# Kernel optimization log

Measured on AMD Instinct MI355X. Metric: run time of the kernel, lower is better.

Reference implementation:

```python
import jax, jax.numpy as jnp
import numpy as np

N = 50000        # number of amino_acid nodes
E = 250000       # edges per relation
HID = 64         # resid_hidden_dim (per-head out dim)
H = 4            # num_heads
L = 2            # resid_num_layers
IN_DIM = 256     # input_dim (fc_dim output)
SCALE = 1.0 / np.sqrt(HID)
EPS_BN = 1e-5


def setup_inputs() -> dict:
    key = jax.random.key(0)
    ks = jax.random.split(key, 12)
    inp = {"x": jax.random.normal(ks[0], (N, HID), jnp.float32)}
    for i, nm in enumerate(("seq", "knn", "dis")):
        inp[f"src_{nm}"] = jax.random.randint(ks[1 + 2 * i], (E,), 0, N, dtype=jnp.int32)
        inp[f"dst_{nm}"] = jax.random.randint(ks[2 + 2 * i], (E,), 0, N, dtype=jnp.int32)
    s = 0.05
    inp["Wsrc"] = jax.random.normal(ks[7], (L, 3, HID, H * HID), jnp.float32) * s
    inp["Wdst"] = jax.random.normal(ks[8], (L, 3, HID, H * HID), jnp.float32) * s
    inp["Wfc"] = jax.random.normal(ks[9], (L, HID, HID), jnp.float32) * s
    inp["bfc"] = jnp.zeros((L, HID), jnp.float32)
    inp["gamma"] = jnp.ones((L, HID), jnp.float32)
    inp["beta"] = jnp.zeros((L, HID), jnp.float32)
    inp["Wdim"] = jax.random.normal(ks[10], (HID, IN_DIM), jnp.float32) * s
    inp["bdim"] = jnp.zeros((IN_DIM,), jnp.float32)
    return inp


def _gat_dot(x, Wsrc, Wdst, src, dst):
    # GATDotConv: q/k projections, scaled dot-product attention per edge,
    # edge-softmax over incoming edges per destination, sum aggregation.
    fs = (x @ Wsrc).reshape(N, H, HID)   # key/value (source) features
    fd = (x @ Wdst).reshape(N, H, HID)   # query (destination) features
    e = jnp.einsum("ehd,ehd->eh", fs[src], fd[dst]) * SCALE   # [E, H]
    m = jax.ops.segment_max(e, dst, num_segments=N)           # [N, H]
    m = jnp.where(jnp.isfinite(m), m, 0.0)                    # zero-in-degree safe
    p = jnp.exp(e - m[dst])
    denom = jax.ops.segment_sum(p, dst, num_segments=N)       # [N, H]
    alpha = p / jnp.maximum(denom[dst], 1e-9)                 # [E, H]
    return jax.ops.segment_sum(fs[src] * alpha[:, :, None], dst, num_segments=N)  # [N, H, HID]


def _batchnorm(x, gamma, beta):
    mu = jnp.mean(x, axis=0)
    var = jnp.var(x, axis=0)
    return gamma * (x - mu) * jax.lax.rsqrt(var + EPS_BN) + beta


def reference(x, src_seq, dst_seq, src_knn, dst_knn, src_dis, dst_dis,
              Wsrc, Wdst, Wfc, bfc, gamma, beta, Wdim, bdim):
    edges = ((src_seq, dst_seq), (src_knn, dst_knn), (src_dis, dst_dis))
    h = x
    for l in range(L):
        # HeteroGraphConv with aggregate='sum' over the three relations
        agg = jnp.zeros((N, H, HID), h.dtype)
        for r in range(3):
            agg = agg + _gat_dot(h, Wsrc[l, r], Wdst[l, r], edges[r][0], edges[r][1])
        h = jnp.mean(agg, axis=1)                       # mean over heads -> [N, HID]
        h = _batchnorm(jax.nn.relu(h @ Wfc[l] + bfc[l]), gamma[l], beta[l])
        # dropout omitted (identity in eval / deterministic reference)
    return h @ Wdim + bdim                              # [N, IN_DIM]
```

## Files before the change

kernel.cpp:

```cpp
#include <hip/hip_runtime.h>
#include <math.h>

#define N_NODES 50000
#define E_EDGES 250000
#define HID 64
#define HD 256
#define L_LAYERS 2
#define IN_DIM_ 256
#define ATT_SCALE 0.125f
#define LOG2E 1.44269504f
#define EPS_BN 1e-5f
#define GX 782

#define PACK_REL (6 * 512 * 64)
#define PACK_FC  (2 * 64 * 64)
#define PACK_DIM (256 * 64)
#define HIST_B   2930
#define PACK_B   864
#define CVT_B    3125
#define PROJ_B   (GX * 3)

#define NBUCK 782
#define P2_B  (3 * NBUCK)
#define BCSTR 32
#define BCAP  512

#define TS 72

typedef __attribute__((ext_vector_type(8))) short bf16x8;
typedef __attribute__((ext_vector_type(4))) float f32x4;

static __device__ __forceinline__ unsigned short f2bf(float f) {
    unsigned u = __float_as_uint(f);
    unsigned r = (u + 0x7fff + ((u >> 16) & 1)) >> 16;
    return (unsigned short)r;
}
static __device__ __forceinline__ float bf2f(unsigned u) {
    return __uint_as_float(u << 16);
}

static __device__ __forceinline__ float rowsum16(float x) {
    int t;
    t = __builtin_amdgcn_update_dpp(0, __float_as_int(x), 0xB1, 0xf, 0xf, true);
    x += __int_as_float(t);
    t = __builtin_amdgcn_update_dpp(0, __float_as_int(x), 0x4E, 0xf, 0xf, true);
    x += __int_as_float(t);
    t = __builtin_amdgcn_update_dpp(0, __float_as_int(x), 0x141, 0xf, 0xf, true);
    x += __int_as_float(t);
    t = __builtin_amdgcn_update_dpp(0, __float_as_int(x), 0x140, 0xf, 0xf, true);
    x += __int_as_float(t);
    return x;
}


__global__ __launch_bounds__(256) void u1_kernel(
        const int* __restrict__ s0, const int* __restrict__ d0,
        const int* __restrict__ s1, const int* __restrict__ d1,
        const int* __restrict__ s2, const int* __restrict__ d2,
        int* __restrict__ bcur, unsigned* __restrict__ ebuf,
        const float* __restrict__ Wsrc, const float* __restrict__ Wdst,
        const float* __restrict__ Wfc, const float* __restrict__ Wdim,
        unsigned short* __restrict__ WtRel, unsigned short* __restrict__ WtFc,
        unsigned short* __restrict__ WtDim,
        const float* __restrict__ x, unsigned short* __restrict__ xb) {
    int b = blockIdx.x;
    if (b < HIST_B) {
        int i = b * 256 + threadIdx.x;
        if (i < 3 * E_EDGES) {
            int r = i / E_EDGES;
            int e = i - r * E_EDGES;
            const int* src = (r == 0) ? s0 : ((r == 1) ? s1 : s2);
            const int* dst = (r == 0) ? d0 : ((r == 1) ? d1 : d2);
            int d = dst[e], s = src[e];
            int bk = r * NBUCK + (d >> 6);
            int pos = atomicAdd(&bcur[(size_t)bk * BCSTR], 1);
            if (pos < BCAP)
                ebuf[(size_t)bk * BCAP + pos] = (unsigned)d | ((unsigned)s << 16);
        }
    } else if (b < HIST_B + PACK_B) {
        int i = (b - HIST_B) * 256 + threadIdx.x;
        if (i < PACK_REL) {
            int k = i & 63;
            int n = (i >> 6) & 511;
            int lr = i >> 15;
            const float* srcm = (n < 256) ? Wsrc : Wdst;
            WtRel[i] = f2bf(srcm[((size_t)lr * 64 + k) * 256 + (n & 255)]);
        } else if (i < PACK_REL + PACK_FC) {
            int j = i - PACK_REL;
            int l = j >> 12, rem = j & 4095;
            int k = rem & 63, n = rem >> 6;
            WtFc[j] = f2bf(Wfc[(size_t)l * 4096 + k * 64 + n]);
        } else if (i < PACK_REL + PACK_FC + PACK_DIM) {
            int j = i - PACK_REL - PACK_FC;
            int k = j & 63, n = j >> 6;
            WtDim[j] = f2bf(Wdim[(size_t)k * 256 + n]);
        }
    } else {
        int i = ((b - HIST_B - PACK_B) * 256 + threadIdx.x) * 4;
        if (i < N_NODES * HID) {
            float4 v = *(const float4*)(x + i);
            uint2 o;
            o.x = (unsigned)f2bf(v.x) | ((unsigned)f2bf(v.y) << 16);
            o.y = (unsigned)f2bf(v.z) | ((unsigned)f2bf(v.w) << 16);
            *(uint2*)(xb + i) = o;
        }
    }
}


__global__ __launch_bounds__(1024) void bscan_kernel(const int* __restrict__ bcur,
                                                     int* __restrict__ bstart,
                                                     int* __restrict__ row_off) {
    __shared__ int A[1024], B[1024];
    int tid = threadIdx.x;
    int r = blockIdx.x;
    int v = (tid < NBUCK) ? bcur[(size_t)(r * NBUCK + tid) * BCSTR] : 0;
    if (v > BCAP) v = BCAP;
    A[tid] = v;
    __syncthreads();
    int* s = A; int* d = B;
    for (int o = 1; o < 1024; o <<= 1) {
        int x = s[tid];
        if (tid >= o) x += s[tid - o];
        d[tid] = x;
        __syncthreads();
        int* t = s; s = d; d = t;
    }
    if (tid < NBUCK) bstart[r * NBUCK + tid] = s[tid] - v;
    if (tid == 0) row_off[(size_t)r * (N_NODES + 1) + N_NODES] = E_EDGES;
}


static __device__ __forceinline__ void proj_body8(int bx,
        const unsigned short* __restrict__ hB, const unsigned short* __restrict__ Wt,
        unsigned short* __restrict__ out, int M, unsigned short* tile) {
    int tid = threadIdx.x;
    int wave = tid >> 6, lane = tid & 63;
    int q = lane >> 4, li = lane & 15;
    int nodeLoc = (wave >> 1) * 32;
    int featLoc = (wave & 1) * 32;
    int nodeBase = bx * 64 + nodeLoc;

    bf16x8 bfr[2][2];
    #pragma unroll
    for (int t = 0; t < 2; ++t) {
        int node = nodeBase + t * 16 + li; if (node >= M) node = M - 1;
        const unsigned short* bp = hB + (size_t)node * 64 + q * 8;
        #pragma unroll
        for (int s = 0; s < 2; ++s) bfr[t][s] = *(const bf16x8*)(bp + s * 32);
    }

    #pragma unroll
    for (int py = 0; py < 8; ++py) {
        int featBase = py * 64 + featLoc;
        bf16x8 afr[2][2];
        #pragma unroll
        for (int t = 0; t < 2; ++t) {
            const unsigned short* ap = Wt + (size_t)(featBase + t * 16 + li) * 64 + q * 8;
            #pragma unroll
            for (int s = 0; s < 2; ++s) afr[t][s] = *(const bf16x8*)(ap + s * 32);
        }
        f32x4 acc[2][2];
        #pragma unroll
        for (int a = 0; a < 2; ++a)
            #pragma unroll
            for (int bq = 0; bq < 2; ++bq)
                #pragma unroll
                for (int i = 0; i < 4; ++i) acc[a][bq][i] = 0.f;
        #pragma unroll
        for (int s = 0; s < 2; ++s)
            #pragma unroll
            for (int ft = 0; ft < 2; ++ft)
                #pragma unroll
                for (int nt = 0; nt < 2; ++nt)
                    acc[ft][nt] = __builtin_amdgcn_mfma_f32_16x16x32_bf16(afr[ft][s], bfr[nt][s], acc[ft][nt], 0, 0, 0);

        #pragma unroll
        for (int ft = 0; ft < 2; ++ft) {
            int fl = featLoc + ft * 16 + q * 4;
            #pragma unroll
            for (int nt = 0; nt < 2; ++nt) {
                int nl = nodeLoc + nt * 16 + li;
                unsigned lo = (unsigned)f2bf(acc[ft][nt][0]) | ((unsigned)f2bf(acc[ft][nt][1]) << 16);
                unsigned hi = (unsigned)f2bf(acc[ft][nt][2]) | ((unsigned)f2bf(acc[ft][nt][3]) << 16);
                uint2 pk; pk.x = lo; pk.y = hi;
                *(uint2*)(tile + nl * TS + fl) = pk;
            }
        }
        __syncthreads();
        #pragma unroll
        for (int p = 0; p < 2; ++p) {
            int idx = p * 256 + tid;
            int nl = idx >> 3, sg = idx & 7;
            int node = bx * 64 + nl;
            if (node < M) {
                uint4 v = *(const uint4*)(tile + nl * TS + sg * 8);
                *(uint4*)(out + (size_t)node * 512 + py * 64 + sg * 8) = v;
            }
        }
        __syncthreads();
    }
}


__global__ __launch_bounds__(256) void u2b_kernel(
        const int* __restrict__ bstart, const int* __restrict__ bcur,
        const unsigned* __restrict__ ebuf, int* __restrict__ csr_src,
        int* __restrict__ row_off,
        const unsigned short* __restrict__ xb, const unsigned short* __restrict__ WtRel0,
        unsigned short* __restrict__ p0, unsigned short* __restrict__ p1,
        unsigned short* __restrict__ p2) {
    __shared__ __align__(16) unsigned short tile[64 * TS];
    __shared__ int cnt64[64], cur64[64];
    int b = blockIdx.x;
    int tid = threadIdx.x;
    if (b < P2_B) {
        int r = b / NBUCK, bk = b - r * NBUCK;
        int n0 = bk << 6;
        int base = bstart[r * NBUCK + bk];
        int cnt = bcur[(size_t)(r * NBUCK + bk) * BCSTR];
        if (cnt > BCAP) cnt = BCAP;
        if (tid < 64) cnt64[tid] = 0;
        __syncthreads();
        const unsigned* eb = ebuf + (size_t)(r * NBUCK + bk) * BCAP;
        for (int t = tid; t < cnt; t += 256)
            atomicAdd(&cnt64[(eb[t] & 0xffff) - n0], 1);
        __syncthreads();
        if (tid < 64) {
            int x = cnt64[tid];
            int incl = x;
            #pragma unroll
            for (int o = 1; o < 64; o <<= 1) {
                int y = __shfl_up(incl, o, 64);
                if (tid >= o) incl += y;
            }
            int excl = incl - x;
            cur64[tid] = excl;
            int node = n0 + tid;
            if (node < N_NODES)
                row_off[(size_t)r * (N_NODES + 1) + node] = base + excl;
        }
        __syncthreads();
        int* cs = csr_src + (size_t)r * E_EDGES + base;
        for (int t = tid; t < cnt; t += 256) {
            unsigned v = eb[t];
            int d = (v & 0xffff) - n0;
            int s = (int)(v >> 16);
            int pos = atomicAdd(&cur64[d], 1);
            cs[pos] = s;
        }
    } else {
        int b2 = b - P2_B;
        int px = b2 % GX;
        int pz = b2 / GX;
        unsigned short* out = (pz == 0) ? p0 : ((pz == 1) ? p1 : p2);
        proj_body8(px, xb, WtRel0 + (size_t)pz * 512 * 64, out, N_NODES, tile);
    }
}

__global__ __launch_bounds__(256) void gemm_proj3(const unsigned short* __restrict__ hB,
                                                  const unsigned short* __restrict__ WtL,
                                                  unsigned short* __restrict__ p0,
                                                  unsigned short* __restrict__ p1,
                                                  unsigned short* __restrict__ p2,
                                                  int M) {
    __shared__ __align__(16) unsigned short tile[64 * TS];
    int r = blockIdx.z;
    unsigned short* out = (r == 0) ? p0 : ((r == 1) ? p1 : p2);
    proj_body8(blockIdx.x, hB, WtL + (size_t)r * 512 * 64, out, M, tile);
}

__global__ __launch_bounds__(256) void gemm_f32out(const unsigned short* __restrict__ hB,
                                                   const unsigned short* __restrict__ Wt,
                                                   const float* __restrict__ bias,
                                                   float* __restrict__ out,
                                                   int M, int Nout, int relu) {
    int tid = threadIdx.x;
    int wave = tid >> 6, lane = tid & 63;
    int q = lane >> 4, li = lane & 15;
    int nodeBase = blockIdx.x * 64 + (wave >> 1) * 32;
    int featBase = blockIdx.y * 64 + (wave & 1) * 32;

    const unsigned short* aptr[2];
    const unsigned short* bptr[2];
    #pragma unroll
    for (int t = 0; t < 2; ++t) {
        aptr[t] = Wt + (size_t)(featBase + t * 16 + li) * 64 + q * 8;
        int node = nodeBase + t * 16 + li; if (node >= M) node = M - 1;
        bptr[t] = hB + (size_t)node * 64 + q * 8;
    }
    f32x4 acc[2][2];
    #pragma unroll
    for (int a = 0; a < 2; ++a)
        #pragma unroll
        for (int bq = 0; bq < 2; ++bq)
            #pragma unroll
            for (int i = 0; i < 4; ++i) acc[a][bq][i] = 0.f;

    #pragma unroll
    for (int s = 0; s < 2; ++s) {
        bf16x8 a[2], b[2];
        #pragma unroll
        for (int t = 0; t < 2; ++t) {
            a[t] = *(const bf16x8*)(aptr[t] + s * 32);
            b[t] = *(const bf16x8*)(bptr[t] + s * 32);
        }
        #pragma unroll
        for (int ft = 0; ft < 2; ++ft)
            #pragma unroll
            for (int nt = 0; nt < 2; ++nt)
                acc[ft][nt] = __builtin_amdgcn_mfma_f32_16x16x32_bf16(a[ft], b[nt], acc[ft][nt], 0, 0, 0);
    }
    #pragma unroll
    for (int ft = 0; ft < 2; ++ft) {
        int f0 = featBase + ft * 16 + q * 4;
        float b0 = bias[f0], b1 = bias[f0 + 1], b2 = bias[f0 + 2], b3 = bias[f0 + 3];
        #pragma unroll
        for (int nt = 0; nt < 2; ++nt) {
            int node = nodeBase + nt * 16 + li;
            if (node >= M) continue;
            float4 o;
            o.x = acc[ft][nt][0] + b0; o.y = acc[ft][nt][1] + b1;
            o.z = acc[ft][nt][2] + b2; o.w = acc[ft][nt][3] + b3;
            if (relu) {
                o.x = fmaxf(o.x, 0.f); o.y = fmaxf(o.y, 0.f);
                o.z = fmaxf(o.z, 0.f); o.w = fmaxf(o.w, 0.f);
            }
            *(float4*)(out + (size_t)node * Nout + f0) = o;
        }
    }
}


#define AGG_ISSUE8(R, sv, j0, cnt, proj) do {                                   \
    _Pragma("unroll")                                                           \
    for (int t_ = 0; t_ < 8; ++t_) {                                            \
        if (t_ < (cnt)) {                                                       \
            int idx_ = __shfl((sv), (j0) + t_, 64);                             \
            (R)[t_] = *(const uint2*)((proj) + (size_t)idx_ * 512 + lane * 4);  \
        }                                                                       \
    }                                                                           \
} while (0)

#define AGG_PROC8(R, cnt) do {                                                  \
    _Pragma("unroll")                                                           \
    for (int t_ = 0; t_ < 8; ++t_) {                                            \
        if (t_ < (cnt)) {                                                       \
            float s0_ = __uint_as_float((R)[t_].x << 16);                       \
            float s1_ = __uint_as_float((R)[t_].x & 0xffff0000u);               \
            float s2_ = __uint_as_float((R)[t_].y << 16);                       \
            float s3_ = __uint_as_float((R)[t_].y & 0xffff0000u);               \
            float p_ = s0_ * fd0_ + s1_ * fd1_ + s2_ * fd2_ + s3_ * fd3_;       \
            p_ = rowsum16(p_);                                                  \
            p_ = fminf(fmaxf(p_, -60.f), 60.f);                                 \
            float pe_ = __builtin_amdgcn_exp2f(p_);                             \
            den_ += pe_;                                                        \
            a0_ += pe_ * s0_; a1_ += pe_ * s1_;                                 \
            a2_ += pe_ * s2_; a3_ += pe_ * s3_;                                 \
        }                                                                       \
    }                                                                           \
} while (0)

#define AGG_REL(proj, fdr, sv, deg, cs, rv, cB) do {                            \
    if ((deg) > 0) {                                                            \
        float fd0_ = bf2f((fdr).x & 0xffff) * FS;                               \
        float fd1_ = __uint_as_float((fdr).x & 0xffff0000u) * FS;               \
        float fd2_ = bf2f((fdr).y & 0xffff) * FS;                               \
        float fd3_ = __uint_as_float((fdr).y & 0xffff0000u) * FS;               \
        float den_ = 0.f, a0_ = 0.f, a1_ = 0.f, a2_ = 0.f, a3_ = 0.f;           \
        AGG_PROC8(rv, cB);                                                      \
        int e_ = (cB);                                                          \
        int sv_ = (sv);                                                         \
        while (e_ < (deg)) {                                                    \
            if ((e_ & 63) == 0) {                                               \
                int o_ = e_ + lane;                                             \
                sv_ = (o_ < (deg)) ? (cs)[o_] : 0;                              \
            }                                                                   \
            int nt_ = (deg) - e_; if (nt_ > 8) nt_ = 8;                         \
            uint2 rt_[8];                                                       \
            AGG_ISSUE8(rt_, sv_, (e_ & 63), nt_, proj);                         \
            AGG_PROC8(rt_, nt_);                                                \
            e_ += nt_;                                                          \
        }                                                                       \
        float inv_ = 1.0f / fmaxf(den_, 1e-9f);                                 \
        t0 += a0_ * inv_; t1 += a1_ * inv_;                                     \
        t2 += a2_ * inv_; t3 += a3_ * inv_;                                     \
    }                                                                           \
} while (0)

__global__ __launch_bounds__(256) void agg_fused(const int* __restrict__ row_off,
                                                 const int* __restrict__ csr_src,
                                                 const unsigned short* __restrict__ p0,
                                                 const unsigned short* __restrict__ p1,
                                                 const unsigned short* __restrict__ p2,
                                                 unsigned short* __restrict__ hm) {
    int wave = (blockIdx.x * 256 + threadIdx.x) >> 6;
    int lane = threadIdx.x & 63;
    if (wave >= N_NODES) return;
    int dst = wave;
    const float FS = ATT_SCALE * LOG2E;

    const int* ro0 = row_off;
    const int* ro1 = row_off + (N_NODES + 1);
    const int* ro2 = row_off + 2 * (N_NODES + 1);
    int b0 = ro0[dst], e0 = ro0[dst + 1];
    int b1 = ro1[dst], e1 = ro1[dst + 1];
    int b2 = ro2[dst], e2 = ro2[dst + 1];
    uint2 fdr0 = *(const uint2*)(p0 + (size_t)dst * 512 + 256 + lane * 4);
    uint2 fdr1 = *(const uint2*)(p1 + (size_t)dst * 512 + 256 + lane * 4);
    uint2 fdr2 = *(const uint2*)(p2 + (size_t)dst * 512 + 256 + lane * 4);
    int deg0 = e0 - b0, deg1 = e1 - b1, deg2 = e2 - b2;

    const int* cs0 = csr_src + b0;
    const int* cs1 = csr_src + E_EDGES + b1;
    const int* cs2 = csr_src + 2 * E_EDGES + b2;
    int sv0 = (lane < deg0) ? cs0[lane] : 0;
    int sv1 = (lane < deg1) ? cs1[lane] : 0;
    int sv2 = (lane < deg2) ? cs2[lane] : 0;

    uint2 rv0[8], rv1[8], rv2[8];
    int c0 = deg0 < 8 ? deg0 : 8;
    int c1 = deg1 < 8 ? deg1 : 8;
    int c2 = deg2 < 8 ? deg2 : 8;
    AGG_ISSUE8(rv0, sv0, 0, c0, p0);
    AGG_ISSUE8(rv1, sv1, 0, c1, p1);
    AGG_ISSUE8(rv2, sv2, 0, c2, p2);

    float t0 = 0.f, t1 = 0.f, t2 = 0.f, t3 = 0.f;
    AGG_REL(p0, fdr0, sv0, deg0, cs0, rv0, c0);
    AGG_REL(p1, fdr1, sv1, deg1, cs1, rv1, c1);
    AGG_REL(p2, fdr2, sv2, deg2, cs2, rv2, c2);

    t0 += __shfl_xor(t0, 16, 64); t0 += __shfl_xor(t0, 32, 64);
    t1 += __shfl_xor(t1, 16, 64); t1 += __shfl_xor(t1, 32, 64);
    t2 += __shfl_xor(t2, 16, 64); t2 += __shfl_xor(t2, 32, 64);
    t3 += __shfl_xor(t3, 16, 64); t3 += __shfl_xor(t3, 32, 64);
    if (lane < 16) {
        unsigned lo = (unsigned)f2bf(t0 * 0.25f) | ((unsigned)f2bf(t1 * 0.25f) << 16);
        unsigned hi = (unsigned)f2bf(t2 * 0.25f) | ((unsigned)f2bf(t3 * 0.25f) << 16);
        uint2 pk; pk.x = lo; pk.y = hi;
        *(uint2*)(hm + (size_t)dst * 64 + lane * 4) = pk;
    }
}


__global__ __launch_bounds__(256) void bn_reduce_kernel(const float* __restrict__ y,
                                                        float* __restrict__ acc1,
                                                        float* __restrict__ acc2) {
    int tid = threadIdx.x;
    int c = tid & 63;
    int g = tid >> 6;
    int rowStart = blockIdx.x * 4 + g;
    int stride = gridDim.x * 4;
    float s1 = 0.f, s2 = 0.f;
    for (int r = rowStart; r < N_NODES; r += stride) {
        float v = y[(size_t)r * 64 + c];
        s1 += v; s2 += v * v;
    }
    __shared__ float l1[4][64], l2[4][64];
    l1[g][c] = s1; l2[g][c] = s2;
    __syncthreads();
    if (g == 0) {
        s1 = l1[0][c] + l1[1][c] + l1[2][c] + l1[3][c];
        s2 = l2[0][c] + l2[1][c] + l2[2][c] + l2[3][c];
        atomicAdd(&acc1[c], s1);
        atomicAdd(&acc2[c], s2);
    }
}

__global__ void bn_apply_kernel(const float* __restrict__ y, const float* __restrict__ acc1,
                                const float* __restrict__ acc2, const float* __restrict__ gamma,
                                const float* __restrict__ beta,
                                unsigned short* __restrict__ outb) {
    int i = blockIdx.x * blockDim.x + threadIdx.x;
    if (i >= N_NODES * HID) return;
    int c = i & 63;
    const float invN = 1.0f / (float)N_NODES;
    float mu = acc1[c] * invN;
    float var = acc2[c] * invN - mu * mu;
    float v = gamma[c] * (y[i] - mu) * rsqrtf(var + EPS_BN) + beta[c];
    outb[i] = f2bf(v);
}


extern "C" void kernel_launch(void* const* d_in, const int* in_sizes, int n_in,
                              void* d_out, int out_size, void* d_ws, size_t ws_size,
                              hipStream_t stream) {
    const float* x     = (const float*)d_in[0];
    const int* srcs[3] = {(const int*)d_in[1], (const int*)d_in[3], (const int*)d_in[5]};
    const int* dsts[3] = {(const int*)d_in[2], (const int*)d_in[4], (const int*)d_in[6]};
    const float* Wsrc  = (const float*)d_in[7];
    const float* Wdst  = (const float*)d_in[8];
    const float* Wfc   = (const float*)d_in[9];
    const float* bfc   = (const float*)d_in[10];
    const float* gamma = (const float*)d_in[11];
    const float* beta  = (const float*)d_in[12];
    const float* Wdim  = (const float*)d_in[13];
    const float* bdim  = (const float*)d_in[14];
    float* out = (float*)d_out;

    char* ws = (char*)d_ws;
    size_t off = 0;
    auto alloc = [&](size_t bytes) -> void* {
        void* p = ws + off;
        off += (bytes + 255) & ~(size_t)255;
        return p;
    };
    float* bnacc  = (float*)alloc(256 * 4);
    int* bcur     = (int*)alloc((size_t)3 * NBUCK * BCSTR * 4);
    int* bstart   = (int*)alloc((size_t)3 * NBUCK * 4);
    int* row_off  = (int*)alloc((size_t)3 * (N_NODES + 1) * 4);
    int* csr_src  = (int*)alloc((size_t)3 * E_EDGES * 4);
    unsigned* ebuf = (unsigned*)alloc((size_t)3 * NBUCK * BCAP * 4);
    unsigned short* proj0 = (unsigned short*)alloc((size_t)N_NODES * 512 * 2);
    unsigned short* proj1 = (unsigned short*)alloc((size_t)N_NODES * 512 * 2);
    unsigned short* proj2 = (unsigned short*)alloc((size_t)N_NODES * 512 * 2);
    unsigned short* hm    = (unsigned short*)alloc((size_t)N_NODES * HID * 2);
    float* ybuf           = (float*)alloc((size_t)N_NODES * HID * 4);
    unsigned short* xb    = (unsigned short*)alloc((size_t)N_NODES * HID * 2);
    unsigned short* hb0   = (unsigned short*)alloc((size_t)N_NODES * HID * 2);
    unsigned short* hb1   = (unsigned short*)alloc((size_t)N_NODES * HID * 2);
    unsigned short* WtRel = (unsigned short*)alloc((size_t)PACK_REL * 2);
    unsigned short* WtFc  = (unsigned short*)alloc((size_t)PACK_FC * 2);
    unsigned short* WtDim = (unsigned short*)alloc((size_t)PACK_DIM * 2);

    hipMemsetAsync(bnacc, 0, 1024 + (size_t)3 * NBUCK * BCSTR * 4, stream);

    u1_kernel<<<HIST_B + PACK_B + CVT_B, 256, 0, stream>>>(
        srcs[0], dsts[0], srcs[1], dsts[1], srcs[2], dsts[2],
        bcur, ebuf, Wsrc, Wdst, Wfc, Wdim, WtRel, WtFc, WtDim, x, xb);

    bscan_kernel<<<3, 1024, 0, stream>>>(bcur, bstart, row_off);

    u2b_kernel<<<P2_B + PROJ_B, 256, 0, stream>>>(
        bstart, bcur, ebuf, csr_src, row_off, xb, WtRel, proj0, proj1, proj2);

    unsigned short* hbufs[2] = {hb0, hb1};
    const unsigned short* hcur = xb;
    for (int l = 0; l < L_LAYERS; ++l) {
        if (l > 0) {
            dim3 g(GX, 1, 3);
            gemm_proj3<<<g, 256, 0, stream>>>(hcur, WtRel + (size_t)l * 3 * 512 * 64,
                                              proj0, proj1, proj2, N_NODES);
        }
        agg_fused<<<(N_NODES + 3) / 4, 256, 0, stream>>>(row_off, csr_src,
                                                         proj0, proj1, proj2, hm);
        dim3 g2(GX, 1);
        gemm_f32out<<<g2, 256, 0, stream>>>(hm, WtFc + (size_t)l * 64 * 64, bfc + (size_t)l * HID,
                                            ybuf, N_NODES, 64, 1);
        float* ba = bnacc + l * 128;
        bn_reduce_kernel<<<256, 256, 0, stream>>>(ybuf, ba, ba + 64);
        bn_apply_kernel<<<(N_NODES * HID + 255) / 256, 256, 0, stream>>>(
            ybuf, ba, ba + 64, gamma + (size_t)l * HID, beta + (size_t)l * HID, hbufs[l]);
        hcur = hbufs[l];
    }
    dim3 g3(GX, IN_DIM_ / 64);
    gemm_f32out<<<g3, 256, 0, stream>>>(hcur, WtDim, bdim, out, N_NODES, IN_DIM_, 0);
}
```

Measured before the change: 483.2 us.

## Fuse batchnorm statistics into FC GEMM and apply BN in consumer GEMMs

Computes the per-channel batchnorm sums and sums of squares in the FC GEMM epilogue, using row reductions and atomics spread over 8 partial slots. The separate reduce and apply kernels and the bf16 hidden buffers are removed. The next layer's projection and the final output GEMM now read the fp32 activations, apply the normalization in their load path and convert to bf16 there. The final GEMM also reuses each node tile across all four output column blocks. This removes two kernels per layer and one full pass over the activations, at the cost of redundant BN coefficient setup in every block and atomic contention on the stats slots.

After: 476.0 us (median of 2 runs). No clear change (-1.5%).

```diff
diff --git a/kernel.cpp b/kernel.cpp
--- a/kernel.cpp
+++ b/kernel.cpp
@@ -4,7 +4,6 @@
 #define N_NODES 50000
 #define E_EDGES 250000
 #define HID 64
-#define HD 256
 #define L_LAYERS 2
 #define IN_DIM_ 256
 #define ATT_SCALE 0.125f
@@ -131,24 +130,14 @@
 }
 
 
-static __device__ __forceinline__ void proj_body8(int bx,
-        const unsigned short* __restrict__ hB, const unsigned short* __restrict__ Wt,
+static __device__ __forceinline__ void proj_core(int bx, const bf16x8 bfr[2][2],
+        const unsigned short* __restrict__ Wt,
         unsigned short* __restrict__ out, int M, unsigned short* tile) {
     int tid = threadIdx.x;
     int wave = tid >> 6, lane = tid & 63;
     int q = lane >> 4, li = lane & 15;
     int nodeLoc = (wave >> 1) * 32;
     int featLoc = (wave & 1) * 32;
-    int nodeBase = bx * 64 + nodeLoc;
-
-    bf16x8 bfr[2][2];
-    #pragma unroll
-    for (int t = 0; t < 2; ++t) {
-        int node = nodeBase + t * 16 + li; if (node >= M) node = M - 1;
-        const unsigned short* bp = hB + (size_t)node * 64 + q * 8;
-        #pragma unroll
-        for (int s = 0; s < 2; ++s) bfr[t][s] = *(const bf16x8*)(bp + s * 32);
-    }
 
     #pragma unroll
     for (int py = 0; py < 8; ++py) {
@@ -201,6 +190,68 @@
         __syncthreads();
     }
 }
+
+static __device__ __forceinline__ void load_bfr_bf16(int bx,
+        const unsigned short* __restrict__ hB, int M, bf16x8 bfr[2][2]) {
+    int tid = threadIdx.x;
+    int wave = tid >> 6, lane = tid & 63;
+    int q = lane >> 4, li = lane & 15;
+    int nodeBase = bx * 64 + (wave >> 1) * 32;
+    #pragma unroll
+    for (int t = 0; t < 2; ++t) {
+        int node = nodeBase + t * 16 + li; if (node >= M) node = M - 1;
+        const unsigned short* bp = hB + (size_t)node * 64 + q * 8;
+        #pragma unroll
+        for (int s = 0; s < 2; ++s) bfr[t][s] = *(const bf16x8*)(bp + s * 32);
+    }
+}
+
+static __device__ __forceinline__ void load_bfr_bn(int bx,
+        const float* __restrict__ y, int M,
+        const float* s_a, const float* s_b, bf16x8 bfr[2][2]) {
+    int tid = threadIdx.x;
+    int wave = tid >> 6, lane = tid & 63;
+    int q = lane >> 4, li = lane & 15;
+    int nodeBase = bx * 64 + (wave >> 1) * 32;
+    #pragma unroll
+    for (int t = 0; t < 2; ++t) {
+        int node = nodeBase + t * 16 + li; if (node >= M) node = M - 1;
+        const float* bp = y + (size_t)node * 64 + q * 8;
+        #pragma unroll
+        for (int s = 0; s < 2; ++s) {
+            int fb = q * 8 + s * 32;
+            float4 u0 = *(const float4*)(bp + s * 32);
+            float4 u1 = *(const float4*)(bp + s * 32 + 4);
+            bf16x8 v;
+            v[0] = (short)f2bf(u0.x * s_a[fb + 0] + s_b[fb + 0]);
+            v[1] = (short)f2bf(u0.y * s_a[fb + 1] + s_b[fb + 1]);
+            v[2] = (short)f2bf(u0.z * s_a[fb + 2] + s_b[fb + 2]);
+            v[3] = (short)f2bf(u0.w * s_a[fb + 3] + s_b[fb + 3]);
+            v[4] = (short)f2bf(u1.x * s_a[fb + 4] + s_b[fb + 4]);
+            v[5] = (short)f2bf(u1.y * s_a[fb + 5] + s_b[fb + 5]);
+            v[6] = (short)f2bf(u1.z * s_a[fb + 6] + s_b[fb + 6]);
+            v[7] = (short)f2bf(u1.w * s_a[fb + 7] + s_b[fb + 7]);
+            bfr[t][s] = v;
+        }
+    }
+}
+
+#define BN_PREAMBLE(stats, gamma, beta, s_a, s_b) do {                          \
+    int tid_ = threadIdx.x;                                                     \
+    if (tid_ < 64) {                                                            \
+        float s1_ = 0.f, s2_ = 0.f;                                             \
+        _Pragma("unroll")                                                       \
+        for (int c_ = 0; c_ < 8; ++c_) {                                        \
+            s1_ += (stats)[c_ * 128 + tid_];                                    \
+            s2_ += (stats)[c_ * 128 + 64 + tid_];                               \
+        }                                                                       \
+        float mu_ = s1_ * (1.f / N_NODES);                                      \
+        float var_ = s2_ * (1.f / N_NODES) - mu_ * mu_;                         \
+        float a_ = (gamma)[tid_] * rsqrtf(var_ + EPS_BN);                       \
+        (s_a)[tid_] = a_; (s_b)[tid_] = (beta)[tid_] - mu_ * a_;                \
+    }                                                                           \
+    __syncthreads();                                                            \
+} while (0)
 
 
 __global__ __launch_bounds__(256) void u2b_kernel(
@@ -254,32 +305,39 @@
         int px = b2 % GX;
         int pz = b2 / GX;
         unsigned short* out = (pz == 0) ? p0 : ((pz == 1) ? p1 : p2);
-        proj_body8(px, xb, WtRel0 + (size_t)pz * 512 * 64, out, N_NODES, tile);
-    }
-}
-
-__global__ __launch_bounds__(256) void gemm_proj3(const unsigned short* __restrict__ hB,
-                                                  const unsigned short* __restrict__ WtL,
-                                                  unsigned short* __restrict__ p0,
-                                                  unsigned short* __restrict__ p1,
-                                                  unsigned short* __restrict__ p2,
-                                                  int M) {
+        bf16x8 bfr[2][2];
+        load_bfr_bf16(px, xb, N_NODES, bfr);
+        proj_core(px, bfr, WtRel0 + (size_t)pz * 512 * 64, out, N_NODES, tile);
+    }
+}
+
+__global__ __launch_bounds__(256) void proj_bn_kernel(
+        const float* __restrict__ y, const float* __restrict__ stats,
+        const float* __restrict__ gamma, const float* __restrict__ beta,
+        const unsigned short* __restrict__ WtL,
+        unsigned short* __restrict__ p0, unsigned short* __restrict__ p1,
+        unsigned short* __restrict__ p2, int M) {
     __shared__ __align__(16) unsigned short tile[64 * TS];
+    __shared__ float s_a[64], s_b[64];
+    BN_PREAMBLE(stats, gamma, beta, s_a, s_b);
+    bf16x8 bfr[2][2];
+    load_bfr_bn(blockIdx.x, y, M, s_a, s_b, bfr);
     int r = blockIdx.z;
     unsigned short* out = (r == 0) ? p0 : ((r == 1) ? p1 : p2);
-    proj_body8(blockIdx.x, hB, WtL + (size_t)r * 512 * 64, out, M, tile);
-}
-
-__global__ __launch_bounds__(256) void gemm_f32out(const unsigned short* __restrict__ hB,
-                                                   const unsigned short* __restrict__ Wt,
-                                                   const float* __restrict__ bias,
-                                                   float* __restrict__ out,
-                                                   int M, int Nout, int relu) {
+    proj_core(blockIdx.x, bfr, WtL + (size_t)r * 512 * 64, out, M, tile);
+}
+
+
+__global__ __launch_bounds__(256) void fc_bn_kernel(
+        const unsigned short* __restrict__ hB,
+        const unsigned short* __restrict__ Wt,
+        const float* __restrict__ bias,
+        float* __restrict__ y, float* __restrict__ stats, int M) {
     int tid = threadIdx.x;
     int wave = tid >> 6, lane = tid & 63;
     int q = lane >> 4, li = lane & 15;
     int nodeBase = blockIdx.x * 64 + (wave >> 1) * 32;
-    int featBase = blockIdx.y * 64 + (wave & 1) * 32;
+    int featBase = (wave & 1) * 32;
 
     const unsigned short* aptr[2];
     const unsigned short* bptr[2];
@@ -311,6 +369,8 @@
             for (int nt = 0; nt < 2; ++nt)
                 acc[ft][nt] = __builtin_amdgcn_mfma_f32_16x16x32_bf16(a[ft], b[nt], acc[ft][nt], 0, 0, 0);
     }
+    float st1[2][4] = {{0.f,0.f,0.f,0.f},{0.f,0.f,0.f,0.f}};
+    float st2[2][4] = {{0.f,0.f,0.f,0.f},{0.f,0.f,0.f,0.f}};
     #pragma unroll
     for (int ft = 0; ft < 2; ++ft) {
         int f0 = featBase + ft * 16 + q * 4;
@@ -318,15 +378,93 @@
         #pragma unroll
         for (int nt = 0; nt < 2; ++nt) {
             int node = nodeBase + nt * 16 + li;
-            if (node >= M) continue;
             float4 o;
-            o.x = acc[ft][nt][0] + b0; o.y = acc[ft][nt][1] + b1;
-            o.z = acc[ft][nt][2] + b2; o.w = acc[ft][nt][3] + b3;
-            if (relu) {
-                o.x = fmaxf(o.x, 0.f); o.y = fmaxf(o.y, 0.f);
-                o.z = fmaxf(o.z, 0.f); o.w = fmaxf(o.w, 0.f);
+            o.x = fmaxf(acc[ft][nt][0] + b0, 0.f);
+            o.y = fmaxf(acc[ft][nt][1] + b1, 0.f);
+            o.z = fmaxf(acc[ft][nt][2] + b2, 0.f);
+            o.w = fmaxf(acc[ft][nt][3] + b3, 0.f);
+            if (node < M) {
+                *(float4*)(y + (size_t)node * 64 + f0) = o;
+                st1[ft][0] += o.x; st1[ft][1] += o.y; st1[ft][2] += o.z; st1[ft][3] += o.w;
+                st2[ft][0] += o.x * o.x; st2[ft][1] += o.y * o.y;
+                st2[ft][2] += o.z * o.z; st2[ft][3] += o.w * o.w;
             }
-            *(float4*)(out + (size_t)node * Nout + f0) = o;
+        }
+    }
+    #pragma unroll
+    for (int ft = 0; ft < 2; ++ft)
+        #pragma unroll
+        for (int j = 0; j < 4; ++j) {
+            st1[ft][j] = rowsum16(st1[ft][j]);
+            st2[ft][j] = rowsum16(st2[ft][j]);
+        }
+    if (li == 0) {
+        float* st = stats + (blockIdx.x & 7) * 128;
+        #pragma unroll
+        for (int ft = 0; ft < 2; ++ft) {
+            int f0 = featBase + ft * 16 + q * 4;
+            #pragma unroll
+            for (int j = 0; j < 4; ++j) {
+                atomicAdd(&st[f0 + j], st1[ft][j]);
+                atomicAdd(&st[64 + f0 + j], st2[ft][j]);
+            }
+        }
+    }
+}
+
+
+__global__ __launch_bounds__(256) void gemm_fin_bn(
+        const float* __restrict__ y, const float* __restrict__ stats,
+        const float* __restrict__ gamma, const float* __restrict__ beta,
+        const unsigned short* __restrict__ Wt, const float* __restrict__ bias,
+        float* __restrict__ out, int M) {
+    __shared__ float s_a[64], s_b[64];
+    BN_PREAMBLE(stats, gamma, beta, s_a, s_b);
+    int tid = threadIdx.x;
+    int wave = tid >> 6, lane = tid & 63;
+    int q = lane >> 4, li = lane & 15;
+    int nodeBase = blockIdx.x * 64 + (wave >> 1) * 32;
+
+    bf16x8 bfr[2][2];
+    load_bfr_bn(blockIdx.x, y, M, s_a, s_b, bfr);
+
+    #pragma unroll
+    for (int by = 0; by < 4; ++by) {
+        int featBase = by * 64 + (wave & 1) * 32;
+        bf16x8 afr[2][2];
+        #pragma unroll
+        for (int t = 0; t < 2; ++t) {
+            const unsigned short* ap = Wt + (size_t)(featBase + t * 16 + li) * 64 + q * 8;
+            #pragma unroll
+            for (int s = 0; s < 2; ++s) afr[t][s] = *(const bf16x8*)(ap + s * 32);
+        }
+        f32x4 acc[2][2];
+        #pragma unroll
+        for (int a = 0; a < 2; ++a)
+            #pragma unroll
+            for (int bq = 0; bq < 2; ++bq)
+                #pragma unroll
+                for (int i = 0; i < 4; ++i) acc[a][bq][i] = 0.f;
+        #pragma unroll
+        for (int s = 0; s < 2; ++s)
+            #pragma unroll
+            for (int ft = 0; ft < 2; ++ft)
+                #pragma unroll
+                for (int nt = 0; nt < 2; ++nt)
+                    acc[ft][nt] = __builtin_amdgcn_mfma_f32_16x16x32_bf16(afr[ft][s], bfr[nt][s], acc[ft][nt], 0, 0, 0);
+        #pragma unroll
+        for (int ft = 0; ft < 2; ++ft) {
+            int f0 = featBase + ft * 16 + q * 4;
+            float b0 = bias[f0], b1 = bias[f0 + 1], b2 = bias[f0 + 2], b3 = bias[f0 + 3];
+            #pragma unroll
+            for (int nt = 0; nt < 2; ++nt) {
+                int node = nodeBase + nt * 16 + li;
+                if (node >= M) continue;
+                float4 o;
+                o.x = acc[ft][nt][0] + b0; o.y = acc[ft][nt][1] + b1;
+                o.z = acc[ft][nt][2] + b2; o.w = acc[ft][nt][3] + b3;
+                *(float4*)(out + (size_t)node * IN_DIM_ + f0) = o;
+            }
         }
     }
 }
@@ -444,45 +582,6 @@
 }
 
 
-__global__ __launch_bounds__(256) void bn_reduce_kernel(const float* __restrict__ y,
-                                                        float* __restrict__ acc1,
-                                                        float* __restrict__ acc2) {
-    int tid = threadIdx.x;
-    int c = tid & 63;
-    int g = tid >> 6;
-    int rowStart = blockIdx.x * 4 + g;
-    int stride = gridDim.x * 4;
-    float s1 = 0.f, s2 = 0.f;
-    for (int r = rowStart; r < N_NODES; r += stride) {
-        float v = y[(size_t)r * 64 + c];
-        s1 += v; s2 += v * v;
-    }
-    __shared__ float l1[4][64], l2[4][64];
-    l1[g][c] = s1; l2[g][c] = s2;
-    __syncthreads();
-    if (g == 0) {
-        s1 = l1[0][c] + l1[1][c] + l1[2][c] + l1[3][c];
-        s2 = l2[0][c] + l2[1][c] + l2[2][c] + l2[3][c];
-        atomicAdd(&acc1[c], s1);
-        atomicAdd(&acc2[c], s2);
-    }
-}
-
-__global__ void bn_apply_kernel(const float* __restrict__ y, const float* __restrict__ acc1,
-                                const float* __restrict__ acc2, const float* __restrict__ gamma,
-                                const float* __restrict__ beta,
-                                unsigned short* __restrict__ outb) {
-    int i = blockIdx.x * blockDim.x + threadIdx.x;
-    if (i >= N_NODES * HID) return;
-    int c = i & 63;
-    const float invN = 1.0f / (float)N_NODES;
-    float mu = acc1[c] * invN;
-    float var = acc2[c] * invN - mu * mu;
-    float v = gamma[c] * (y[i] - mu) * rsqrtf(var + EPS_BN) + beta[c];
-    outb[i] = f2bf(v);
-}
-
-
 extern "C" void kernel_launch(void* const* d_in, const int* in_sizes, int n_in,
                               void* d_out, int out_size, void* d_ws, size_t ws_size,
                               hipStream_t stream) {
@@ -506,7 +605,7 @@
         off += (bytes + 255) & ~(size_t)255;
         return p;
     };
-    float* bnacc  = (float*)alloc(256 * 4);
+    float* stats8 = (float*)alloc((size_t)2 * 8 * 128 * 4);
     int* bcur     = (int*)alloc((size_t)3 * NBUCK * BCSTR * 4);
     int* bstart   = (int*)alloc((size_t)3 * NBUCK * 4);
     int* row_off  = (int*)alloc((size_t)3 * (N_NODES + 1) * 4);
@@ -518,13 +617,11 @@
     unsigned short* hm    = (unsigned short*)alloc((size_t)N_NODES * HID * 2);
     float* ybuf           = (float*)alloc((size_t)N_NODES * HID * 4);
     unsigned short* xb    = (unsigned short*)alloc((size_t)N_NODES * HID * 2);
-    unsigned short* hb0   = (unsigned short*)alloc((size_t)N_NODES * HID * 2);
-    unsigned short* hb1   = (unsigned short*)alloc((size_t)N_NODES * HID * 2);
     unsigned short* WtRel = (unsigned short*)alloc((size_t)PACK_REL * 2);
     unsigned short* WtFc  = (unsigned short*)alloc((size_t)PACK_FC * 2);
     unsigned short* WtDim = (unsigned short*)alloc((size_t)PACK_DIM * 2);
 
-    hipMemsetAsync(bnacc, 0, 1024 + (size_t)3 * NBUCK * BCSTR * 4, stream);
+    hipMemsetAsync(stats8, 0, (size_t)2 * 8 * 128 * 4 + (size_t)3 * NBUCK * BCSTR * 4, stream);
 
     u1_kernel<<<HIST_B + PACK_B + CVT_B, 256, 0, stream>>>(
         srcs[0], dsts[0], srcs[1], dsts[1], srcs[2], dsts[2],
@@ -535,25 +632,19 @@
     u2b_kernel<<<P2_B + PROJ_B, 256, 0, stream>>>(
         bstart, bcur, ebuf, csr_src, row_off, xb, WtRel, proj0, proj1, proj2);
 
-    unsigned short* hbufs[2] = {hb0, hb1};
-    const unsigned short* hcur = xb;
-    for (int l = 0; l < L_LAYERS; ++l) {
-        if (l > 0) {
-            dim3 g(GX, 1, 3);
-            gemm_proj3<<<g, 256, 0, stream>>>(hcur, WtRel + (size_t)l * 3 * 512 * 64,
-                                              proj0, proj1, proj2, N_NODES);
-        }
-        agg_fused<<<(N_NODES + 3) / 4, 256, 0, stream>>>(row_off, csr_src,
-                                                         proj0, proj1, proj2, hm);
-        dim3 g2(GX, 1);
-        gemm_f32out<<<g2, 256, 0, stream>>>(hm, WtFc + (size_t)l * 64 * 64, bfc + (size_t)l * HID,
-                                            ybuf, N_NODES, 64, 1);
-        float* ba = bnacc + l * 128;
-        bn_reduce_kernel<<<256, 256, 0, stream>>>(ybuf, ba, ba + 64);
-        bn_apply_kernel<<<(N_NODES * HID + 255) / 256, 256, 0, stream>>>(
-            ybuf, ba, ba + 64, gamma + (size_t)l * HID, beta + (size_t)l * HID, hbufs[l]);
-        hcur = hbufs[l];
-    }
-    dim3 g3(GX, IN_DIM_ / 64);
-    gemm_f32out<<<g3, 256, 0, stream>>>(hcur, WtDim, bdim, out, N_NODES, IN_DIM_, 0);
-}
+    agg_fused<<<(N_NODES + 3) / 4, 256, 0, stream>>>(row_off, csr_src,
+                                                     proj0, proj1, proj2, hm);
+    fc_bn_kernel<<<GX, 256, 0, stream>>>(hm, WtFc, bfc, ybuf, stats8, N_NODES);
+
+    dim3 g(GX, 1, 3);
+    proj_bn_kernel<<<g, 256, 0, stream>>>(ybuf, stats8, gamma, beta,
+                                          WtRel + (size_t)3 * 512 * 64,
+                                          proj0, proj1, proj2, N_NODES);
+    agg_fused<<<(N_NODES + 3) / 4, 256, 0, stream>>>(row_off, csr_src,
+                                                     proj0, proj1, proj2, hm);
+    fc_bn_kernel<<<GX, 256, 0, stream>>>(hm, WtFc + (size_t)64 * 64, bfc + HID,
+                                         ybuf, stats8 + 8 * 128, N_NODES);
+
+    gemm_fin_bn<<<GX, 256, 0, stream>>>(ybuf, stats8 + 8 * 128, gamma + HID, beta + HID,
+                                        WtDim, bdim, out, N_NODES);
+}
```
